# Optimization experiments

Hardware: AMD Instinct MI355X
Metric: run time of the kernel (lower is better)

## Reference

```python
import jax, jax.numpy as jnp
import numpy as np

HEADS = 4
DIM_HEAD = 32
DIM = 128
EPS = 1e-12  # F.normalize eps


def _rmsnorm(t, g):
    # F.normalize over channel dim (dim=1), then * g * sqrt(dim)
    n = jnp.sqrt(jnp.sum(t * t, axis=1, keepdims=True))
    return t / jnp.maximum(n, EPS) * g * (DIM ** 0.5)


def setup_inputs() -> dict:
    key = jax.random.key(0)
    ks = jax.random.split(key, 5)
    b, H, W = 16, 96, 96
    x = jax.random.normal(ks[0], (b, DIM, H, W), dtype=jnp.float32)
    norm_g = jnp.ones((1, DIM, 1, 1), dtype=jnp.float32)
    qkv_w = jax.random.normal(ks[1], (3 * HEADS * DIM_HEAD, DIM), dtype=jnp.float32) * 0.05
    mem_kv = jax.random.normal(ks[2], (2, HEADS, DIM_HEAD, 4), dtype=jnp.float32)
    out_w = jax.random.normal(ks[3], (DIM, HEADS * DIM_HEAD), dtype=jnp.float32) * 0.05
    out_b = jnp.zeros((DIM,), dtype=jnp.float32)
    out_norm_g = jnp.ones((1, DIM, 1, 1), dtype=jnp.float32)
    return {"x": x, "norm_g": norm_g, "qkv_w": qkv_w, "mem_kv": mem_kv,
            "out_w": out_w, "out_b": out_b, "out_norm_g": out_norm_g}


def reference(x, norm_g, qkv_w, mem_kv, out_w, out_b, out_norm_g):
    b, c, H, W = x.shape
    n = H * W
    scale = DIM_HEAD ** (-0.5)

    xn = _rmsnorm(x, norm_g)
    # 1x1 conv (no bias) == channel GEMM
    qkv = jnp.einsum('oc,bchw->bohw', qkv_w, xn)  # [b, 3*h*d, H, W]
    q, k, v = jnp.split(qkv, 3, axis=1)

    def to_heads(t):
        return t.reshape(b, HEADS, DIM_HEAD, n)  # b h d n

    q, k, v = to_heads(q), to_heads(k), to_heads(v)

    mk = jnp.broadcast_to(mem_kv[0], (b, HEADS, DIM_HEAD, mem_kv.shape[-1]))
    mv = jnp.broadcast_to(mem_kv[1], (b, HEADS, DIM_HEAD, mem_kv.shape[-1]))
    k = jnp.concatenate([mk, k], axis=-1)
    v = jnp.concatenate([mv, v], axis=-1)

    q = jax.nn.softmax(q, axis=-2) * scale  # softmax over d
    k = jax.nn.softmax(k, axis=-1)          # softmax over n

    context = jnp.einsum('bhdn,bhen->bhde', k, v)  # [b,h,d,d]
    out = jnp.einsum('bhde,bhdn->bhen', context, q)  # [b,h,d,n]
    out = out.reshape(b, HEADS * DIM_HEAD, H, W)

    out = jnp.einsum('oc,bchw->bohw', out_w, out) + out_b[None, :, None, None]
    return _rmsnorm(out, out_norm_g)
```

## Files before the change

kernel.cpp:

```cpp
#include <hip/hip_runtime.h>
#include <hip/hip_bf16.h>
#include <math.h>

#define NPIX 9216
#define NBLK 48
#define TPB 6
#define NTILE 288
#define SCALE 0.17677669529663687f
#define SQRT128 11.313708498984761f

typedef __attribute__((ext_vector_type(8))) short short8;
typedef __attribute__((ext_vector_type(4))) float f32x4;

static __device__ __forceinline__ unsigned short f2bf(float f) {
  return __bfloat16_as_ushort(__float2bfloat16(f));
}
static __device__ __forceinline__ float bf2f(unsigned short h) {
  return __bfloat162float(__ushort_as_bfloat16(h));
}


__global__ __launch_bounds__(256) void k_prep2(
    const float* __restrict__ qkv_w, const float* __restrict__ norm_g,
    const float* __restrict__ out_w,
    unsigned short* __restrict__ wbf2, unsigned short* __restrict__ owb2) {
  const int i = blockIdx.x * 256 + threadIdx.x;
  if (i < 6144) {
    const int g = i >> 6, lane = i & 63;
    const int wv = g / 24, rem = g % 24;
    const int mt = rem >> 2, ks = rem & 3;
    const int row = (mt >> 1) * 128 + wv * 32 + (mt & 1) * 16 + (lane & 15);
    const int col = ks * 32 + (lane >> 4) * 8;
    const float* src = qkv_w + row * 128 + col;
    const float* gg = norm_g + col;
    uint4 o;
    o.x = (unsigned)f2bf(src[0] * gg[0]) | ((unsigned)f2bf(src[1] * gg[1]) << 16);
    o.y = (unsigned)f2bf(src[2] * gg[2]) | ((unsigned)f2bf(src[3] * gg[3]) << 16);
    o.z = (unsigned)f2bf(src[4] * gg[4]) | ((unsigned)f2bf(src[5] * gg[5]) << 16);
    o.w = (unsigned)f2bf(src[6] * gg[6]) | ((unsigned)f2bf(src[7] * gg[7]) << 16);
    *(uint4*)(wbf2 + (size_t)i * 8) = o;
  } else if (i < 8192) {
    const int i2 = i - 6144;
    const int g = i2 >> 6, lane = i2 & 63;
    const int wv = g >> 3, rem = g & 7;
    const int mt = rem >> 2, ks = rem & 3;
    const int row = 32 * wv + mt * 16 + (lane & 15);
    const int col = ks * 32 + (lane >> 4) * 8;
    const float* src = out_w + row * 128 + col;
    uint4 o;
    o.x = (unsigned)f2bf(src[0]) | ((unsigned)f2bf(src[1]) << 16);
    o.y = (unsigned)f2bf(src[2]) | ((unsigned)f2bf(src[3]) << 16);
    o.z = (unsigned)f2bf(src[4]) | ((unsigned)f2bf(src[5]) << 16);
    o.w = (unsigned)f2bf(src[6]) | ((unsigned)f2bf(src[7]) << 16);
    *(uint4*)(owb2 + (size_t)i2 * 8) = o;
  }
}

__global__ __launch_bounds__(256) void k_init(const float* __restrict__ mem_kv,
                                              float* __restrict__ ctxG,
                                              float* __restrict__ sumexpG) {
  const int bh = blockIdx.x;
  const int h = bh & 3;
  const float* mk = mem_kv + h * 128;
  const float* mv = mem_kv + 512 + h * 128;
  const int t = threadIdx.x;
  const int d = t >> 3, e0 = (t & 7) * 4;
  float ek[4], se = 0.f;
#pragma unroll
  for (int j = 0; j < 4; ++j) { ek[j] = __expf(mk[d * 4 + j]); se += ek[j]; }
#pragma unroll
  for (int ei = 0; ei < 4; ++ei) {
    const int e = e0 + ei;
    float s = 0.f;
#pragma unroll
    for (int j = 0; j < 4; ++j) s += ek[j] * mv[e * 4 + j];
    ctxG[(bh * 32 + d) * 32 + e] = s;
  }
  if ((t & 7) == 0) sumexpG[bh * 32 + d] = se;
}

template <bool WSQ>
__global__ __launch_bounds__(256, 3) void k1(
    const float* __restrict__ x, const unsigned short* __restrict__ wbf2,
    unsigned short* __restrict__ qb16, float* __restrict__ qf32,
    float* __restrict__ ctx_dst, float* __restrict__ se_dst) {
  __shared__ __align__(16) unsigned char smem[30720 + 17408 + 4096];
  unsigned short* qkv = (unsigned short*)smem;
  unsigned short* xnT0 = (unsigned short*)(smem + 30720);
  float* redu0 = (float*)(smem + 30720 + 17408);

  const int t = threadIdx.x;
  const int b = blockIdx.y;
  const int blk = blockIdx.x;
  const int wv = t >> 6;
  const int lane = t & 63;
  const int lr = lane & 15;
  const int lg = lane >> 4;
  const int r = t >> 3, c4 = (t & 7) * 4;
  const float* xb = x + ((size_t)b * 128) * NPIX + blk * TPB * 32;
  unsigned short* qkv_w = qkv + wv * 96 * 40;

  f32x4 ctx[2][2];
#pragma unroll
  for (int i = 0; i < 2; ++i)
#pragma unroll
    for (int j = 0; j < 2; ++j)
#pragma unroll
      for (int q = 0; q < 4; ++q) ctx[i][j][q] = 0.f;
  float se_row[2] = {0.f, 0.f};

  float4 pf[4];
#pragma unroll
  for (int pass = 0; pass < 4; ++pass)
    pf[pass] = *(const float4*)(xb + (size_t)(pass * 32 + r) * NPIX + c4);

  for (int it = 0; it < TPB; ++it) {
    const int tile = blk * TPB + it;
    unsigned short* xnT = xnT0 + (it & 1) * 4352;
    float* redu = redu0 + (it & 1) * 512;

    {
      float ss0 = 0.f, ss1 = 0.f, ss2 = 0.f, ss3 = 0.f;
#pragma unroll
      for (int pass = 0; pass < 4; ++pass) {
        const int row = pass * 32 + r;
        const float4 v = pf[pass];
        xnT[(c4 + 0) * 136 + row] = f2bf(v.x);
        xnT[(c4 + 1) * 136 + row] = f2bf(v.y);
        xnT[(c4 + 2) * 136 + row] = f2bf(v.z);
        xnT[(c4 + 3) * 136 + row] = f2bf(v.w);
        ss0 = fmaf(v.x, v.x, ss0); ss1 = fmaf(v.y, v.y, ss1);
        ss2 = fmaf(v.z, v.z, ss2); ss3 = fmaf(v.w, v.w, ss3);
      }
      ss0 += __shfl_xor(ss0, 8); ss1 += __shfl_xor(ss1, 8);
      ss2 += __shfl_xor(ss2, 8); ss3 += __shfl_xor(ss3, 8);
      if (!(t & 8))
        *(float4*)&redu[(t >> 4) * 32 + c4] = make_float4(ss0, ss1, ss2, ss3);
    }
    __syncthreads();
    float iv0, iv1;
    {
      float invv = 0.f;
      if (lane < 32) {
        float s = 0.f;
#pragma unroll
        for (int g = 0; g < 16; ++g) s += redu[g * 32 + lane];
        invv = SQRT128 / fmaxf(sqrtf(s), 1e-12f);
      }
      iv0 = __shfl(invv, lr);
      iv1 = __shfl(invv, 16 + lr);
    }
    {
      short8 bfr[4][2];
#pragma unroll
      for (int ks = 0; ks < 4; ++ks)
#pragma unroll
        for (int nt = 0; nt < 2; ++nt)
          bfr[ks][nt] = *(const short8*)&xnT[(nt * 16 + lr) * 136 + ks * 32 + lg * 8];
      if (it + 1 < TPB) {
        const float* xb2 = xb + (it + 1) * 32;
#pragma unroll
        for (int pass = 0; pass < 4; ++pass)
          pf[pass] = *(const float4*)(xb2 + (size_t)(pass * 32 + r) * NPIX + c4);
      }
      const unsigned short* wbase = wbf2 + (size_t)(wv * 24) * 512 + lane * 8;
#pragma unroll 2
      for (int mt = 0; mt < 6; ++mt) {
        f32x4 a0 = {0.f, 0.f, 0.f, 0.f};
        f32x4 a1 = {0.f, 0.f, 0.f, 0.f};
#pragma unroll
        for (int ks = 0; ks < 4; ++ks) {
          const short8 af = *(const short8*)(wbase + (size_t)(mt * 4 + ks) * 512);
          a0 = __builtin_amdgcn_mfma_f32_16x16x32_bf16(af, bfr[ks][0], a0, 0, 0, 0);
          a1 = __builtin_amdgcn_mfma_f32_16x16x32_bf16(af, bfr[ks][1], a1, 0, 0, 0);
        }
#pragma unroll
        for (int q = 0; q < 4; ++q) {
          const int row_l = mt * 16 + lg * 4 + q;
          qkv_w[row_l * 40 + lr] = f2bf(a0[q] * iv0);
          qkv_w[row_l * 40 + 16 + lr] = f2bf(a1[q] * iv1);
        }
      }
    }
    {
#pragma unroll
      for (int px = 0; px < 2; ++px) {
        const int p = px * 16 + lr;
        float qv[8];
#pragma unroll
        for (int j = 0; j < 8; ++j) qv[j] = bf2f(qkv_w[(lg * 8 + j) * 40 + p]);
        float m = qv[0];
#pragma unroll
        for (int j = 1; j < 8; ++j) m = fmaxf(m, qv[j]);
        m = fmaxf(m, __shfl_xor(m, 16));
        m = fmaxf(m, __shfl_xor(m, 32));
        float s = 0.f;
#pragma unroll
        for (int j = 0; j < 8; ++j) { qv[j] = __expf(qv[j] - m); s += qv[j]; }
        s += __shfl_xor(s, 16);
        s += __shfl_xor(s, 32);
        const float rs = SCALE / s;
        if (WSQ) {
          uint4 qo;
          qo.x = (unsigned)f2bf(qv[0] * rs) | ((unsigned)f2bf(qv[1] * rs) << 16);
          qo.y = (unsigned)f2bf(qv[2] * rs) | ((unsigned)f2bf(qv[3] * rs) << 16);
          qo.z = (unsigned)f2bf(qv[4] * rs) | ((unsigned)f2bf(qv[5] * rs) << 16);
          qo.w = (unsigned)f2bf(qv[6] * rs) | ((unsigned)f2bf(qv[7] * rs) << 16);
          *(uint4*)(qb16 +
              ((((size_t)(b * NTILE + tile) * 4 + wv) * 2 + px) * 64 + lane) * 8) = qo;
        } else {
          const int c0g = wv * 32 + lg * 8;
#pragma unroll
          for (int j = 0; j < 8; ++j)
            qf32[((size_t)b * 128 + c0g + j) * NPIX + tile * 32 + p] = qv[j] * rs;
        }
      }
      short8 afk[2];
#pragma unroll
      for (int dt = 0; dt < 2; ++dt) {
        const short8 kraw = *(const short8*)&qkv_w[(32 + dt * 16 + lr) * 40 + lg * 8];
        short8 e16;
        float s = 0.f;
#pragma unroll
        for (int j = 0; j < 8; ++j) {
          const float ev = __expf(bf2f((unsigned short)kraw[j]));
          e16[j] = (short)f2bf(ev);
          s += ev;
        }
        afk[dt] = e16;
        s += __shfl_xor(s, 16);
        s += __shfl_xor(s, 32);
        se_row[dt] += s;
      }
#pragma unroll
      for (int dt = 0; dt < 2; ++dt)
#pragma unroll
        for (int et = 0; et < 2; ++et) {
          const short8 bf = *(const short8*)&qkv_w[(64 + et * 16 + lr) * 40 + lg * 8];
          ctx[dt][et] = __builtin_amdgcn_mfma_f32_16x16x32_bf16(afk[dt], bf, ctx[dt][et], 0, 0, 0);
        }
    }
  }

  if (WSQ) {
    float* dst = ctx_dst + ((size_t)(b * NBLK + blk)) * 4096 + wv * 1024;
#pragma unroll
    for (int dt = 0; dt < 2; ++dt)
#pragma unroll
      for (int et = 0; et < 2; ++et)
#pragma unroll
        for (int q = 0; q < 4; ++q)
          dst[(dt * 16 + lg * 4 + q) * 32 + et * 16 + lr] = ctx[dt][et][q];
    if (lg == 0) {
#pragma unroll
      for (int dt = 0; dt < 2; ++dt)
        se_dst[(b * NBLK + blk) * 128 + wv * 32 + dt * 16 + lr] = se_row[dt];
    }
  } else {
#pragma unroll
    for (int dt = 0; dt < 2; ++dt)
#pragma unroll
      for (int et = 0; et < 2; ++et)
#pragma unroll
        for (int q = 0; q < 4; ++q)
          atomicAdd(&ctx_dst[((size_t)b * 128 + wv * 32 + dt * 16 + lg * 4 + q) * 32 + et * 16 + lr],
                    ctx[dt][et][q]);
    if (lg == 0) {
#pragma unroll
      for (int dt = 0; dt < 2; ++dt)
        atomicAdd(&se_dst[b * 128 + wv * 32 + dt * 16 + lr], se_row[dt]);
    }
  }
}

__global__ __launch_bounds__(256) void k_reduce(
    const float* __restrict__ part_ctx, const float* __restrict__ part_se,
    const float* __restrict__ mem_kv, unsigned short* __restrict__ ctxnT) {
  const int bid = blockIdx.x;
  const int b = bid >> 4, h = (bid >> 2) & 3, dq = bid & 3;
  const int t = threadIdx.x;
  const int dd = t >> 5;
  const int d = dq * 8 + dd;
  const int e = t & 31;
  __shared__ float sise[8];

  const float* mk = mem_kv + h * 128 + d * 4;
  const float* mv = mem_kv + 512 + h * 128 + e * 4;
  float ek[4];
  float acc = 0.f;
#pragma unroll
  for (int j = 0; j < 4; ++j) ek[j] = __expf(mk[j]);
#pragma unroll
  for (int j = 0; j < 4; ++j) acc += ek[j] * mv[j];
  const float* src = part_ctx + (size_t)b * NBLK * 4096 + h * 1024 + d * 32 + e;
  for (int p = 0; p < NBLK; ++p) acc += src[(size_t)p * 4096];
  if (e == 0) {
    float se = ek[0] + ek[1] + ek[2] + ek[3];
    const float* sp = part_se + (size_t)b * NBLK * 128 + h * 32 + d;
    for (int p = 0; p < NBLK; ++p) se += sp[(size_t)p * 128];
    sise[dd] = 1.f / se;
  }
  __syncthreads();
  ctxnT[(size_t)(b * 4 + h) * 1024 + e * 32 + d] = f2bf(acc * sise[dd]);
}

__global__ __launch_bounds__(256) void k_norm(
    const float* __restrict__ ctxG, const float* __restrict__ seG,
    unsigned short* __restrict__ ctxnT) {
  const int b = blockIdx.x;
  const int t = threadIdx.x;
  const int h = t >> 6, d = (t >> 1) & 31, e0 = (t & 1) * 16;
  const int r = h * 32 + d;
  const float ise = 1.f / seG[b * 128 + r];
  const float* src = ctxG + ((size_t)b * 128 + r) * 32;
  unsigned short* dst = ctxnT + ((size_t)(b * 4 + h) * 32) * 32;
#pragma unroll
  for (int i = 0; i < 16; ++i)
    dst[(e0 + i) * 32 + d] = f2bf(src[e0 + i] * ise);
}

__global__ __launch_bounds__(256) void k3_ws(
    const unsigned short* __restrict__ ctxnT, const unsigned short* __restrict__ owb2,
    const unsigned short* __restrict__ qbf, const float* __restrict__ out_b,
    const float* __restrict__ out_norm_g, float* __restrict__ out) {
  __shared__ __align__(16) unsigned char smem[8704 + 2048 + 128];
  unsigned short* o1T = (unsigned short*)smem;
  float* redu = (float*)(smem + 8704);
  float* inv = (float*)(smem + 8704 + 2048);

  const int t = threadIdx.x;
  const int b = blockIdx.y;
  const int tile = blockIdx.x;
  const int p0 = tile * 32;
  const int wv = t >> 6;
  const int lane = t & 63;
  const int lr = lane & 15;
  const int lg = lane >> 4;

  {
    f32x4 o1a[2][2];
#pragma unroll
    for (int i = 0; i < 2; ++i)
#pragma unroll
      for (int j = 0; j < 2; ++j)
#pragma unroll
        for (int q = 0; q < 4; ++q) o1a[i][j][q] = 0.f;
    const unsigned short* cbase = ctxnT + (size_t)(b * 4 + wv) * 1024;
    const unsigned short* qb = qbf + (((size_t)(b * NTILE + tile) * 4 + wv) * 2) * 512;
    short8 bq[2];
#pragma unroll
    for (int nt = 0; nt < 2; ++nt)
      bq[nt] = *(const short8*)(qb + (size_t)(nt * 64 + lane) * 8);
#pragma unroll
    for (int mt = 0; mt < 2; ++mt) {
      const short8 af = *(const short8*)(cbase + (mt * 16 + lr) * 32 + lg * 8);
#pragma unroll
      for (int nt = 0; nt < 2; ++nt)
        o1a[mt][nt] = __builtin_amdgcn_mfma_f32_16x16x32_bf16(af, bq[nt], o1a[mt][nt], 0, 0, 0);
    }
#pragma unroll
    for (int mt = 0; mt < 2; ++mt)
#pragma unroll
      for (int nt = 0; nt < 2; ++nt)
#pragma unroll
        for (int q = 0; q < 4; ++q) {
          const int e = wv * 32 + mt * 16 + lg * 4 + q;
          o1T[(nt * 16 + lr) * 136 + e] = f2bf(o1a[mt][nt][q]);
        }
  }
  __syncthreads();
  f32x4 y[2][2];
#pragma unroll
  for (int i = 0; i < 2; ++i)
#pragma unroll
    for (int j = 0; j < 2; ++j)
#pragma unroll
      for (int q = 0; q < 4; ++q) y[i][j][q] = 0.f;
  const unsigned short* wbase = owb2 + (size_t)(wv * 8) * 512 + lane * 8;
#pragma unroll
  for (int mt = 0; mt < 2; ++mt) {
#pragma unroll
    for (int ks = 0; ks < 4; ++ks) {
      const short8 af = *(const short8*)(wbase + (size_t)(mt * 4 + ks) * 512);
#pragma unroll
      for (int nt = 0; nt < 2; ++nt) {
        const short8 bf = *(const short8*)&o1T[(nt * 16 + lr) * 136 + ks * 32 + lg * 8];
        y[mt][nt] = __builtin_amdgcn_mfma_f32_16x16x32_bf16(af, bf, y[mt][nt], 0, 0, 0);
      }
    }
  }
  {
    float ss[2] = {0.f, 0.f};
#pragma unroll
    for (int mt = 0; mt < 2; ++mt)
#pragma unroll
      for (int q = 0; q < 4; ++q) {
        const int row = 32 * wv + mt * 16 + lg * 4 + q;
        const float bb = out_b[row];
#pragma unroll
        for (int nt = 0; nt < 2; ++nt) {
          y[mt][nt][q] += bb;
          ss[nt] = fmaf(y[mt][nt][q], y[mt][nt][q], ss[nt]);
        }
      }
#pragma unroll
    for (int nt = 0; nt < 2; ++nt)
      redu[(wv * 4 + lg) * 32 + nt * 16 + lr] = ss[nt];
  }
  __syncthreads();
  if (t < 32) {
    float s = 0.f;
#pragma unroll
    for (int g = 0; g < 16; ++g) s += redu[g * 32 + t];
    inv[t] = SQRT128 / fmaxf(sqrtf(s), 1e-12f);
  }
  __syncthreads();
  {
    float* ob = out + (size_t)b * 128 * NPIX + p0;
#pragma unroll
    for (int mt = 0; mt < 2; ++mt)
#pragma unroll
      for (int q = 0; q < 4; ++q) {
        const int row = 32 * wv + mt * 16 + lg * 4 + q;
        const float g = out_norm_g[row];
#pragma unroll
        for (int nt = 0; nt < 2; ++nt) {
          const int col = nt * 16 + lr;
          ob[(size_t)row * NPIX + col] = y[mt][nt][q] * inv[col] * g;
        }
      }
  }
}

__global__ __launch_bounds__(256) void k3f(
    const unsigned short* __restrict__ ctxnT, const unsigned short* __restrict__ owb2,
    const float* __restrict__ out_b, const float* __restrict__ out_norm_g,
    float* __restrict__ io) {
  __shared__ __align__(16) unsigned char smem[8704 + 8704 + 2048 + 128];
  unsigned short* qT = (unsigned short*)smem;
  unsigned short* o1T = (unsigned short*)(smem + 8704);
  float* redu = (float*)(smem + 8704 + 8704);
  float* inv = (float*)(smem + 8704 + 8704 + 2048);

  const int t = threadIdx.x;
  const int b = blockIdx.y;
  const int p0 = blockIdx.x * 32;
  const int wv = t >> 6;
  const int lane = t & 63;
  const int lr = lane & 15;
  const int lg = lane >> 4;

  {
    const float* qb = io + (size_t)b * 128 * NPIX + p0;
    const int r = t >> 3, c4 = (t & 7) * 4;
#pragma unroll
    for (int pass = 0; pass < 4; ++pass) {
      const int row = pass * 32 + r;
      const float4 v = *(const float4*)(qb + (size_t)row * NPIX + c4);
      qT[(c4 + 0) * 136 + row] = f2bf(v.x);
      qT[(c4 + 1) * 136 + row] = f2bf(v.y);
      qT[(c4 + 2) * 136 + row] = f2bf(v.z);
      qT[(c4 + 3) * 136 + row] = f2bf(v.w);
    }
  }
  __syncthreads();
  {
    f32x4 o1a[2][2];
#pragma unroll
    for (int i = 0; i < 2; ++i)
#pragma unroll
      for (int j = 0; j < 2; ++j)
#pragma unroll
        for (int q = 0; q < 4; ++q) o1a[i][j][q] = 0.f;
    const unsigned short* cbase = ctxnT + (size_t)(b * 4 + wv) * 1024;
#pragma unroll
    for (int mt = 0; mt < 2; ++mt) {
      const short8 af = *(const short8*)(cbase + (mt * 16 + lr) * 32 + lg * 8);
#pragma unroll
      for (int nt = 0; nt < 2; ++nt) {
        const short8 bf = *(const short8*)&qT[(nt * 16 + lr) * 136 + wv * 32 + lg * 8];
        o1a[mt][nt] = __builtin_amdgcn_mfma_f32_16x16x32_bf16(af, bf, o1a[mt][nt], 0, 0, 0);
      }
    }
#pragma unroll
    for (int mt = 0; mt < 2; ++mt)
#pragma unroll
      for (int nt = 0; nt < 2; ++nt)
#pragma unroll
        for (int q = 0; q < 4; ++q) {
          const int e = wv * 32 + mt * 16 + lg * 4 + q;
          o1T[(nt * 16 + lr) * 136 + e] = f2bf(o1a[mt][nt][q]);
        }
  }
  __syncthreads();
  f32x4 y[2][2];
#pragma unroll
  for (int i = 0; i < 2; ++i)
#pragma unroll
    for (int j = 0; j < 2; ++j)
#pragma unroll
      for (int q = 0; q < 4; ++q) y[i][j][q] = 0.f;
  const unsigned short* wbase = owb2 + (size_t)(wv * 8) * 512 + lane * 8;
#pragma unroll
  for (int mt = 0; mt < 2; ++mt) {
#pragma unroll
    for (int ks = 0; ks < 4; ++ks) {
      const short8 af = *(const short8*)(wbase + (size_t)(mt * 4 + ks) * 512);
#pragma unroll
      for (int nt = 0; nt < 2; ++nt) {
        const short8 bf = *(const short8*)&o1T[(nt * 16 + lr) * 136 + ks * 32 + lg * 8];
        y[mt][nt] = __builtin_amdgcn_mfma_f32_16x16x32_bf16(af, bf, y[mt][nt], 0, 0, 0);
      }
    }
  }
  {
    float ss[2] = {0.f, 0.f};
#pragma unroll
    for (int mt = 0; mt < 2; ++mt)
#pragma unroll
      for (int q = 0; q < 4; ++q) {
        const int row = 32 * wv + mt * 16 + lg * 4 + q;
        const float bb = out_b[row];
#pragma unroll
        for (int nt = 0; nt < 2; ++nt) {
          y[mt][nt][q] += bb;
          ss[nt] = fmaf(y[mt][nt][q], y[mt][nt][q], ss[nt]);
        }
      }
#pragma unroll
    for (int nt = 0; nt < 2; ++nt)
      redu[(wv * 4 + lg) * 32 + nt * 16 + lr] = ss[nt];
  }
  __syncthreads();
  if (t < 32) {
    float s = 0.f;
#pragma unroll
    for (int g = 0; g < 16; ++g) s += redu[g * 32 + t];
    inv[t] = SQRT128 / fmaxf(sqrtf(s), 1e-12f);
  }
  __syncthreads();
  {
    float* ob = io + (size_t)b * 128 * NPIX + p0;
#pragma unroll
    for (int mt = 0; mt < 2; ++mt)
#pragma unroll
      for (int q = 0; q < 4; ++q) {
        const int row = 32 * wv + mt * 16 + lg * 4 + q;
        const float g = out_norm_g[row];
#pragma unroll
        for (int nt = 0; nt < 2; ++nt) {
          const int col = nt * 16 + lr;
          ob[(size_t)row * NPIX + col] = y[mt][nt][q] * inv[col] * g;
        }
      }
  }
}

extern "C" void kernel_launch(void* const* d_in, const int* in_sizes, int n_in,
                              void* d_out, int out_size, void* d_ws, size_t ws_size,
                              hipStream_t stream) {
  const float* x          = (const float*)d_in[0];
  const float* norm_g     = (const float*)d_in[1];
  const float* qkv_w      = (const float*)d_in[2];
  const float* mem_kv     = (const float*)d_in[3];
  const float* out_w      = (const float*)d_in[4];
  const float* out_b      = (const float*)d_in[5];
  const float* out_norm_g = (const float*)d_in[6];
  float* out = (float*)d_out;

  const size_t PC = (size_t)16 * NBLK * 4096;
  const size_t PS = (size_t)16 * NBLK * 128;
  const size_t QB = (size_t)16 * NPIX * 128;
  const size_t need = (PC + PS) * 4 + (49152 + 16384 + 65536 + QB) * 2;

  if (ws_size >= need) {
    float* part_ctx = (float*)d_ws;
    float* part_se  = part_ctx + PC;
    unsigned short* wbf2  = (unsigned short*)(part_se + PS);
    unsigned short* owb2  = wbf2 + 49152;
    unsigned short* ctxnT = owb2 + 16384;
    unsigned short* qbf   = ctxnT + 65536;
    k_prep2<<<32, 256, 0, stream>>>(qkv_w, norm_g, out_w, wbf2, owb2);
    k1<true><<<dim3(NBLK, 16), 256, 0, stream>>>(x, wbf2, qbf, nullptr, part_ctx, part_se);
    k_reduce<<<256, 256, 0, stream>>>(part_ctx, part_se, mem_kv, ctxnT);
    k3_ws<<<dim3(NTILE, 16), 256, 0, stream>>>(ctxnT, owb2, qbf, out_b, out_norm_g, out);
  } else {
    float* ctxG = (float*)d_ws;
    float* seG  = ctxG + 65536;
    unsigned short* wbf2  = (unsigned short*)(seG + 2048);
    unsigned short* owb2  = wbf2 + 49152;
    unsigned short* ctxnT = owb2 + 16384;
    k_prep2<<<32, 256, 0, stream>>>(qkv_w, norm_g, out_w, wbf2, owb2);
    k_init<<<64, 256, 0, stream>>>(mem_kv, ctxG, seG);
    k1<false><<<dim3(NBLK, 16), 256, 0, stream>>>(x, wbf2, nullptr, out, ctxG, seG);
    k_norm<<<16, 256, 0, stream>>>(ctxG, seG, ctxnT);
    k3f<<<dim3(NTILE, 16), 256, 0, stream>>>(ctxnT, owb2, out_b, out_norm_g, out);
  }
}
```

Baseline: 76.51 us.

## Keep Q projection in registers and permute context layout to match

The Q tiles of the QKV projection are now kept in MFMA accumulator registers and softmaxed directly, instead of being written to shared memory as bf16 and read back. Only K and V go through shared memory, which shrinks the LDS footprint and the stores. Because the register layout of Q rows differs from the original channel order, the context matrix and the fallback qT path are written with a matching channel permutation. This also skips a bf16 rounding of Q before its softmax and packs K/V stores into 32-bit writes. The cost is more live registers in k1, which is launch-bounded for 3 blocks per CU.

```diff
diff --git a/kernel.cpp b/kernel.cpp
--- a/kernel.cpp
+++ b/kernel.cpp
@@ -18,6 +18,7 @@
 static __device__ __forceinline__ float bf2f(unsigned short h) {
   return __bfloat162float(__ushort_as_bfloat16(h));
 }
+
 
 
 __global__ __launch_bounds__(256) void k_prep2(
@@ -84,10 +85,10 @@
     const float* __restrict__ x, const unsigned short* __restrict__ wbf2,
     unsigned short* __restrict__ qb16, float* __restrict__ qf32,
     float* __restrict__ ctx_dst, float* __restrict__ se_dst) {
-  __shared__ __align__(16) unsigned char smem[30720 + 17408 + 4096];
-  unsigned short* qkv = (unsigned short*)smem;
-  unsigned short* xnT0 = (unsigned short*)(smem + 30720);
-  float* redu0 = (float*)(smem + 30720 + 17408);
+  __shared__ __align__(16) unsigned char smem[20480 + 17408 + 4096];
+  unsigned short* kv = (unsigned short*)smem;
+  unsigned short* xnT0 = (unsigned short*)(smem + 20480);
+  float* redu0 = (float*)(smem + 20480 + 17408);
 
   const int t = threadIdx.x;
   const int b = blockIdx.y;
@@ -98,7 +99,7 @@
   const int lg = lane >> 4;
   const int r = t >> 3, c4 = (t & 7) * 4;
   const float* xb = x + ((size_t)b * 128) * NPIX + blk * TPB * 32;
-  unsigned short* qkv_w = qkv + wv * 96 * 40;
+  unsigned short* kv_w = kv + wv * 64 * 40;
 
   f32x4 ctx[2][2];
 #pragma unroll
@@ -150,45 +151,41 @@
       iv0 = __shfl(invv, lr);
       iv1 = __shfl(invv, 16 + lr);
     }
+    short8 bfr[4][2];
+#pragma unroll
+    for (int ks = 0; ks < 4; ++ks)
+#pragma unroll
+      for (int nt = 0; nt < 2; ++nt)
+        bfr[ks][nt] = *(const short8*)&xnT[(nt * 16 + lr) * 136 + ks * 32 + lg * 8];
+    if (it + 1 < TPB) {
+      const float* xb2 = xb + (it + 1) * 32;
+#pragma unroll
+      for (int pass = 0; pass < 4; ++pass)
+        pf[pass] = *(const float4*)(xb2 + (size_t)(pass * 32 + r) * NPIX + c4);
+    }
+    const unsigned short* wbase = wbf2 + (size_t)(wv * 24) * 512 + lane * 8;
     {
-      short8 bfr[4][2];
-#pragma unroll
-      for (int ks = 0; ks < 4; ++ks)
-#pragma unroll
-        for (int nt = 0; nt < 2; ++nt)
-          bfr[ks][nt] = *(const short8*)&xnT[(nt * 16 + lr) * 136 + ks * 32 + lg * 8];
-      if (it + 1 < TPB) {
-        const float* xb2 = xb + (it + 1) * 32;
-#pragma unroll
-        for (int pass = 0; pass < 4; ++pass)
-          pf[pass] = *(const float4*)(xb2 + (size_t)(pass * 32 + r) * NPIX + c4);
-      }
-      const unsigned short* wbase = wbf2 + (size_t)(wv * 24) * 512 + lane * 8;
-#pragma unroll 2
-      for (int mt = 0; mt < 6; ++mt) {
-        f32x4 a0 = {0.f, 0.f, 0.f, 0.f};
-        f32x4 a1 = {0.f, 0.f, 0.f, 0.f};
+      f32x4 aq[2][2];
+#pragma unroll
+      for (int i = 0; i < 2; ++i)
+#pragma unroll
+        for (int j = 0; j < 2; ++j)
+#pragma unroll
+          for (int q = 0; q < 4; ++q) aq[i][j][q] = 0.f;
+#pragma unroll
+      for (int mt = 0; mt < 2; ++mt)
 #pragma unroll
         for (int ks = 0; ks < 4; ++ks) {
           const short8 af = *(const short8*)(wbase + (size_t)(mt * 4 + ks) * 512);
-          a0 = __builtin_amdgcn_mfma_f32_16x16x32_bf16(af, bfr[ks][0], a0, 0, 0, 0);
-          a1 = __builtin_amdgcn_mfma_f32_16x16x32_bf16(af, bfr[ks][1], a1, 0, 0, 0);
-        }
-#pragma unroll
-        for (int q = 0; q < 4; ++q) {
-          const int row_l = mt * 16 + lg * 4 + q;
-          qkv_w[row_l * 40 + lr] = f2bf(a0[q] * iv0);
-          qkv_w[row_l * 40 + 16 + lr] = f2bf(a1[q] * iv1);
-        }
-      }
-    }
-    {
-#pragma unroll
-      for (int px = 0; px < 2; ++px) {
-        const int p = px * 16 + lr;
+          aq[mt][0] = __builtin_amdgcn_mfma_f32_16x16x32_bf16(af, bfr[ks][0], aq[mt][0], 0, 0, 0);
+          aq[mt][1] = __builtin_amdgcn_mfma_f32_16x16x32_bf16(af, bfr[ks][1], aq[mt][1], 0, 0, 0);
+        }
+#pragma unroll
+      for (int nt = 0; nt < 2; ++nt) {
+        const float iv = nt ? iv1 : iv0;
         float qv[8];
 #pragma unroll
-        for (int j = 0; j < 8; ++j) qv[j] = bf2f(qkv_w[(lg * 8 + j) * 40 + p]);
+        for (int j = 0; j < 8; ++j) qv[j] = aq[j >> 2][nt][j & 3] * iv;
         float m = qv[0];
 #pragma unroll
         for (int j = 1; j < 8; ++j) m = fmaxf(m, qv[j]);
@@ -207,18 +204,41 @@
           qo.z = (unsigned)f2bf(qv[4] * rs) | ((unsigned)f2bf(qv[5] * rs) << 16);
           qo.w = (unsigned)f2bf(qv[6] * rs) | ((unsigned)f2bf(qv[7] * rs) << 16);
           *(uint4*)(qb16 +
-              ((((size_t)(b * NTILE + tile) * 4 + wv) * 2 + px) * 64 + lane) * 8) = qo;
+              ((((size_t)(b * NTILE + tile) * 4 + wv) * 2 + nt) * 64 + lane) * 8) = qo;
         } else {
-          const int c0g = wv * 32 + lg * 8;
-#pragma unroll
-          for (int j = 0; j < 8; ++j)
-            qf32[((size_t)b * 128 + c0g + j) * NPIX + tile * 32 + p] = qv[j] * rs;
-        }
-      }
+#pragma unroll
+          for (int j = 0; j < 8; ++j) {
+            const int d = (j >> 2) * 16 + lg * 4 + (j & 3);
+            qf32[((size_t)b * 128 + wv * 32 + d) * NPIX + tile * 32 + nt * 16 + lr] = qv[j] * rs;
+          }
+        }
+      }
+    }
+    {
+#pragma unroll 2
+      for (int mt = 2; mt < 6; ++mt) {
+        f32x4 a0 = {0.f, 0.f, 0.f, 0.f};
+        f32x4 a1 = {0.f, 0.f, 0.f, 0.f};
+#pragma unroll
+        for (int ks = 0; ks < 4; ++ks) {
+          const short8 af = *(const short8*)(wbase + (size_t)(mt * 4 + ks) * 512);
+          a0 = __builtin_amdgcn_mfma_f32_16x16x32_bf16(af, bfr[ks][0], a0, 0, 0, 0);
+          a1 = __builtin_amdgcn_mfma_f32_16x16x32_bf16(af, bfr[ks][1], a1, 0, 0, 0);
+        }
+#pragma unroll
+        for (int q = 0; q < 4; ++q) {
+          const int row_l = (mt - 2) * 16 + lg * 4 + q;
+          const unsigned pk = (unsigned)f2bf(a0[q] * iv0)
+                            | ((unsigned)f2bf(a1[q] * iv1) << 16);
+          *(unsigned*)&kv_w[row_l * 40 + lr * 2] = pk;
+        }
+      }
+    }
+    {
       short8 afk[2];
 #pragma unroll
       for (int dt = 0; dt < 2; ++dt) {
-        const short8 kraw = *(const short8*)&qkv_w[(32 + dt * 16 + lr) * 40 + lg * 8];
+        const short8 kraw = *(const short8*)&kv_w[(dt * 16 + lr) * 40 + lg * 8];
         short8 e16;
         float s = 0.f;
 #pragma unroll
@@ -236,7 +256,7 @@
       for (int dt = 0; dt < 2; ++dt)
 #pragma unroll
         for (int et = 0; et < 2; ++et) {
-          const short8 bf = *(const short8*)&qkv_w[(64 + et * 16 + lr) * 40 + lg * 8];
+          const short8 bf = *(const short8*)&kv_w[(32 + et * 16 + lr) * 40 + lg * 8];
           ctx[dt][et] = __builtin_amdgcn_mfma_f32_16x16x32_bf16(afk[dt], bf, ctx[dt][et], 0, 0, 0);
         }
     }
@@ -301,7 +321,8 @@
     sise[dd] = 1.f / se;
   }
   __syncthreads();
-  ctxnT[(size_t)(b * 4 + h) * 1024 + e * 32 + d] = f2bf(acc * sise[dd]);
+  const int c = ((d >> 2) & 3) * 8 + ((d >> 4) & 1) * 4 + (d & 3);
+  ctxnT[(size_t)(b * 4 + h) * 1024 + e * 32 + c] = f2bf(acc * sise[dd]);
 }
 
 __global__ __launch_bounds__(256) void k_norm(
@@ -314,9 +335,10 @@
   const float ise = 1.f / seG[b * 128 + r];
   const float* src = ctxG + ((size_t)b * 128 + r) * 32;
   unsigned short* dst = ctxnT + ((size_t)(b * 4 + h) * 32) * 32;
+  const int c = ((d >> 2) & 3) * 8 + ((d >> 4) & 1) * 4 + (d & 3);
 #pragma unroll
   for (int i = 0; i < 16; ++i)
-    dst[(e0 + i) * 32 + d] = f2bf(src[e0 + i] * ise);
+    dst[(e0 + i) * 32 + c] = f2bf(src[e0 + i] * ise);
 }
 
 __global__ __launch_bounds__(256) void k3_ws(
@@ -456,11 +478,13 @@
 #pragma unroll
     for (int pass = 0; pass < 4; ++pass) {
       const int row = pass * 32 + r;
+      const int dl = row & 31;
+      const int pc = (row & ~31) | (((dl >> 2) & 3) * 8 + ((dl >> 4) & 1) * 4 + (dl & 3));
       const float4 v = *(const float4*)(qb + (size_t)row * NPIX + c4);
-      qT[(c4 + 0) * 136 + row] = f2bf(v.x);
-      qT[(c4 + 1) * 136 + row] = f2bf(v.y);
-      qT[(c4 + 2) * 136 + row] = f2bf(v.z);
-      qT[(c4 + 3) * 136 + row] = f2bf(v.w);
+      qT[(c4 + 0) * 136 + pc] = f2bf(v.x);
+      qT[(c4 + 1) * 136 + pc] = f2bf(v.y);
+      qT[(c4 + 2) * 136 + pc] = f2bf(v.z);
+      qT[(c4 + 3) * 136 + pc] = f2bf(v.w);
     }
   }
   __syncthreads();
```

Measured after the change: 72.81 us. -4.8%, faster.
